# Kernel tuning notes

Measured on AMD Instinct MI355X. Metric: run time of the kernel, lower is better.

Reference implementation:

```python
import jax, jax.numpy as jnp
import numpy as np
from jax import lax

B, C, H, W = 8, 128, 128, 128


def setup_inputs() -> dict:
    key = jax.random.key(0)
    ks = jax.random.split(key, 10)
    s = 0.02
    return {
        "x": jax.random.normal(ks[0], (B, C, H, W), jnp.float32),
        "ln_w": jnp.ones((C,), jnp.float32),
        "ln_b": jnp.zeros((C,), jnp.float32),
        "qkv_w": jax.random.normal(ks[1], (3 * C, C, 1, 1), jnp.float32) * s,
        "qkv_b": jnp.zeros((3 * C,), jnp.float32),
        "dw_w": jax.random.normal(ks[2], (3 * C, 1, 3, 3), jnp.float32) * s,
        "dw_b": jnp.zeros((3 * C,), jnp.float32),
        "proj_w": jax.random.normal(ks[3], (C, C, 1, 1), jnp.float32) * s,
        "proj_b": jnp.zeros((C,), jnp.float32),
        "temp1": jnp.ones((1, 1), jnp.float32),
        "temp2": jnp.ones((1, 1), jnp.float32),
    }


def reference(x, ln_w, ln_b, qkv_w, qkv_b, dw_w, dw_b, proj_w, proj_b, temp1, temp2):
    Cd = x.shape[1]

    def ln(t):  # WithBias LayerNorm over channel dim (unbiased=False var)
        mu = t.mean(axis=1, keepdims=True)
        var = ((t - mu) ** 2).mean(axis=1, keepdims=True)
        return (t - mu) / jnp.sqrt(var + 1e-5) * ln_w[None, :, None, None] + ln_b[None, :, None, None]

    def conv1(t, w, b):  # 1x1 conv
        return jnp.einsum('bchw,oc->bohw', t, w[:, :, 0, 0]) + b[None, :, None, None]

    def dwc(t):  # depthwise 3x3, pad 1
        y = lax.conv_general_dilated(t, dw_w, (1, 1), ((1, 1), (1, 1)),
                                     dimension_numbers=('NCHW', 'OIHW', 'NCHW'),
                                     feature_group_count=t.shape[1])
        return y + dw_b[None, :, None, None]

    def l2n(t):  # F.normalize over last axis, eps=1e-12
        return t / jnp.maximum(jnp.linalg.norm(t, axis=-1, keepdims=True), 1e-12)

    # ---- stage 1: pool over H, attention over W (channel-pooled) ----
    qkv = dwc(conv1(ln(x), qkv_w, qkv_b))
    q1, k1, v1 = qkv[:, :Cd], qkv[:, Cd:2 * Cd], qkv[:, 2 * Cd:]
    q1 = l2n(q1.mean(axis=2)[:, None])           # [B,1,C,W]
    k1 = l2n(k1.max(axis=2)[:, None])            # [B,1,C,W]
    attn1 = jax.nn.softmax(jnp.einsum('bocw,bocv->bowv', q1, k1) * temp1, axis=-1)  # [B,1,W,W]
    out1 = jnp.einsum('bchw,bowv->bchv', v1, attn1)
    out1 = x + conv1(out1, proj_w, proj_b)

    # ---- stage 2: pool over C, attention over H ----
    qkv = dwc(conv1(ln(out1), qkv_w, qkv_b))
    q2, k2, v2 = qkv[:, :Cd], qkv[:, Cd:2 * Cd], qkv[:, 2 * Cd:]
    q2 = l2n(q2.mean(axis=1)[:, None])           # [B,1,H,W]
    k2 = l2n(k2.mean(axis=1)[:, None])           # [B,1,H,W]
    attn2 = jax.nn.softmax(jnp.einsum('bohw,bogw->bohg', q2, k2) * temp2, axis=-1)  # [B,1,H,H]
    out2 = jnp.einsum('bchw,bohg->bcgw', v2, attn2)  # = (v^T @ attn)^T
    out = conv1(out2, proj_w, proj_b) + out1
    return out
```

## Files before the change

### kernel.cpp

```cpp
#include <hip/hip_runtime.h>

typedef __attribute__((ext_vector_type(8))) short bf16x8;
typedef __attribute__((ext_vector_type(4))) float f32x4;
typedef __attribute__((ext_vector_type(4))) unsigned short us4;
typedef __attribute__((ext_vector_type(4))) unsigned int u32x4;

static constexpr int CC = 128, NN = 16384;
static constexpr int O3 = 384;
static constexpr long long CN  = (long long)CC * NN;
static constexpr long long O3N = (long long)O3 * NN;

__device__ __forceinline__ float wave_sum(float v) {
  for (int o = 32; o; o >>= 1) v += __shfl_xor(v, o);
  return v;
}
__device__ __forceinline__ float wave_max(float v) {
  for (int o = 32; o; o >>= 1) v = fmaxf(v, __shfl_xor(v, o));
  return v;
}
__device__ __forceinline__ unsigned short f2bf(float f) {
  unsigned u = __float_as_uint(f);
  u += 0x7FFF + ((u >> 16) & 1);
  return (unsigned short)(u >> 16);
}
__device__ __forceinline__ float bf2f(unsigned short h) {
  return __uint_as_float((unsigned)h << 16);
}

__global__ __launch_bounds__(64) void k_prep(const float* __restrict__ qkvw,
                                             const float* __restrict__ qkvb,
                                             const float* __restrict__ lnw,
                                             const float* __restrict__ lnb,
                                             const float* __restrict__ projw,
                                             unsigned short* __restrict__ Aq,
                                             unsigned short* __restrict__ Ap,
                                             float* __restrict__ Svec,
                                             float* __restrict__ bias2) {
  int o = blockIdx.x, t = threadIdx.x;
  if (o < O3) {
    float w0 = qkvw[o * 128 + t], w1 = qkvw[o * 128 + t + 64];
    unsigned short h0 = f2bf(w0 * lnw[t]), h1 = f2bf(w1 * lnw[t + 64]);
    Aq[o * 128 + t] = h0; Aq[o * 128 + t + 64] = h1;
    float s = wave_sum(bf2f(h0) + bf2f(h1));
    float bs = wave_sum(w0 * lnb[t] + w1 * lnb[t + 64]);
    if (t == 0) { Svec[o] = s; bias2[o] = qkvb[o] + bs; }
  } else {
    int r = o - O3;
    Ap[r * 128 + t] = f2bf(projw[r * 128 + t]);
    Ap[r * 128 + t + 64] = f2bf(projw[r * 128 + t + 64]);
  }
}

__global__ __launch_bounds__(256) void k_stats(const float* __restrict__ in,
                                               float* __restrict__ mu,
                                               float* __restrict__ rs) {
  int p = blockIdx.x * 256 + threadIdx.x;
  int b = p >> 14, n = p & (NN - 1);
  const float* base = in + (size_t)b * CN + n;
  float s1 = 0.f, s2 = 0.f;
#pragma unroll 8
  for (int c = 0; c < CC; ++c) { float v = base[(size_t)c * NN]; s1 += v; s2 += v * v; }
  float m = s1 * (1.f / CC);
  float var = s2 * (1.f / CC) - m * m;
  mu[p] = m;
  rs[p] = rsqrtf(var + 1e-5f);
}

__global__ __launch_bounds__(256) void k_qkv_mfma(
    const float* __restrict__ x, const float* __restrict__ mu, const float* __restrict__ rs,
    const unsigned short* __restrict__ Aq, const float* __restrict__ Svec,
    const float* __restrict__ bias2, unsigned short* __restrict__ out, int b0) {
  __shared__ unsigned short Bs[64 * 136];
  __shared__ unsigned short As[384 * 40];
  int bz = blockIdx.z, bg = b0 + bz;
  int n0 = blockIdx.x * 64;
  int t = threadIdx.x, w = t >> 6, l = t & 63;
  int lr = l & 15, lg = l >> 4;
  const float* xb = x + (size_t)bg * CN + n0;

  {
    int cg = t >> 4, nl = t & 15;
#pragma unroll
    for (int r = 0; r < 8; ++r) {
      int c = r * 16 + cg;
      const float* src = xb + (size_t)c * NN + nl;
#pragma unroll
      for (int q = 0; q < 4; ++q)
        Bs[(nl + q * 16) * 136 + c] = f2bf(src[q * 16]);
    }
  }

  f32x4 acc[6][4];
#pragma unroll
  for (int i = 0; i < 6; ++i)
#pragma unroll
    for (int j = 0; j < 4; ++j) acc[i][j] = (f32x4){0.f, 0.f, 0.f, 0.f};

  const unsigned int* Asrc = (const unsigned int*)Aq;
  unsigned int* Adst = (unsigned int*)As;
  for (int ks = 0; ks < 4; ++ks) {
    __syncthreads();
#pragma unroll
    for (int r = 0; r < 24; ++r) {
      int idx = r * 256 + t;
      int o = idx >> 4, cp = idx & 15;
      Adst[o * 20 + cp] = Asrc[(size_t)o * 64 + ks * 16 + cp];
    }
    __syncthreads();
    bf16x8 bfr[4];
#pragma unroll
    for (int j = 0; j < 4; ++j)
      bfr[j] = *(const bf16x8*)&Bs[(16 * j + lr) * 136 + ks * 32 + lg * 8];
#pragma unroll
    for (int i = 0; i < 6; ++i) {
      bf16x8 afr = *(const bf16x8*)&As[(96 * w + 16 * i + lr) * 40 + lg * 8];
#pragma unroll
      for (int j = 0; j < 4; ++j)
        acc[i][j] = __builtin_amdgcn_mfma_f32_16x16x32_bf16(afr, bfr[j], acc[i][j], 0, 0, 0);
    }
  }

  float rsv[4], muv[4];
#pragma unroll
  for (int j = 0; j < 4; ++j) {
    int n = n0 + 16 * j + lr;
    rsv[j] = rs[(size_t)bg * NN + n];
    muv[j] = mu[(size_t)bg * NN + n];
  }
#pragma unroll
  for (int i = 0; i < 6; ++i) {
    int ob = 96 * w + 16 * i + lg * 4;
    float sv[4], bv[4];
#pragma unroll
    for (int r2 = 0; r2 < 4; ++r2) { sv[r2] = Svec[ob + r2]; bv[r2] = bias2[ob + r2]; }
#pragma unroll
    for (int j = 0; j < 4; ++j) {
      int n = n0 + 16 * j + lr;
      unsigned short* op = out + (size_t)bz * O3N + n;
#pragma unroll
      for (int r2 = 0; r2 < 4; ++r2)
        op[(size_t)(ob + r2) * NN] = f2bf(rsv[j] * (acc[i][j][r2] - muv[j] * sv[r2]) + bv[r2]);
    }
  }
}

__global__ __launch_bounds__(1024) void k_dwc(unsigned short* __restrict__ buf,
                                              const float* __restrict__ dww,
                                              const float* __restrict__ dwb,
                                              float* __restrict__ qm,
                                              float* __restrict__ km,
                                              int b0, int stage) {
  __shared__ unsigned short pl[130 * 144];
  __shared__ float red[32 * 128];
  int o = blockIdx.x, bz = blockIdx.y, bg = b0 + bz;
  int t = threadIdx.x;
  unsigned short* base = buf + (size_t)bz * O3N + (size_t)o * NN;

  for (int i = t; i < 9360; i += 1024) ((unsigned*)pl)[i] = 0u;
  __syncthreads();
#pragma unroll
  for (int r = 0; r < 2; ++r) {
    int idx = r * 1024 + t;
    int row = idx >> 4, c8 = (idx & 15) * 8;
    *(u32x4*)&pl[(row + 1) * 144 + 8 + c8] = *(const u32x4*)&base[row * 128 + c8];
  }
  __syncthreads();

  const float* wg = dww + o * 9;
  float w00 = wg[0], w01 = wg[1], w02 = wg[2];
  float w10 = wg[3], w11 = wg[4], w12 = wg[5];
  float w20 = wg[6], w21 = wg[7], w22 = wg[8];
  float bias = dwb[o];
  int mode = (stage == 0) ? (o < 128 ? 1 : (o < 256 ? 2 : 0)) : 0;
  int hh0 = t >> 5, w0 = (t & 31) * 4;
  float csum[4] = {0.f, 0.f, 0.f, 0.f};
  float cmax[4] = {-1e30f, -1e30f, -1e30f, -1e30f};

#pragma unroll
  for (int g = 0; g < 4; ++g) {
    int h = g * 32 + hh0;
    float a0 = bias, a1 = bias, a2 = bias, a3 = bias;
#pragma unroll
    for (int dr = 0; dr < 3; ++dr) {
      const unsigned short* rp = &pl[(h + dr) * 144];
      us4 cA = *(const us4*)&rp[w0 + 4];
      us4 cB = *(const us4*)&rp[w0 + 8];
      us4 cC = *(const us4*)&rp[w0 + 12];
      float f0 = bf2f(cA[3]), f1 = bf2f(cB[0]), f2 = bf2f(cB[1]);
      float f3 = bf2f(cB[2]), f4 = bf2f(cB[3]), f5 = bf2f(cC[0]);
      float wr0 = (dr == 0) ? w00 : (dr == 1 ? w10 : w20);
      float wr1 = (dr == 0) ? w01 : (dr == 1 ? w11 : w21);
      float wr2 = (dr == 0) ? w02 : (dr == 1 ? w12 : w22);
      a0 += f0 * wr0 + f1 * wr1 + f2 * wr2;
      a1 += f1 * wr0 + f2 * wr1 + f3 * wr2;
      a2 += f2 * wr0 + f3 * wr1 + f4 * wr2;
      a3 += f3 * wr0 + f4 * wr1 + f5 * wr2;
    }
    if (mode == 0) {
      us4 ov;
      ov[0] = f2bf(a0); ov[1] = f2bf(a1); ov[2] = f2bf(a2); ov[3] = f2bf(a3);
      *(us4*)&base[g * 4096 + t * 4] = ov;
    } else if (mode == 1) {
      csum[0] += a0; csum[1] += a1; csum[2] += a2; csum[3] += a3;
    } else {
      cmax[0] = fmaxf(cmax[0], a0); cmax[1] = fmaxf(cmax[1], a1);
      cmax[2] = fmaxf(cmax[2], a2); cmax[3] = fmaxf(cmax[3], a3);
    }
  }

  if (mode) {
    int j = t >> 5;
#pragma unroll
    for (int dx = 0; dx < 4; ++dx)
      red[j * 128 + w0 + dx] = (mode == 1) ? csum[dx] : cmax[dx];
    __syncthreads();
    if (t < 128) {
      float v = red[t];
      if (mode == 1) {
        for (int jj = 1; jj < 32; ++jj) v += red[jj * 128 + t];
        qm[(size_t)bg * NN + o * 128 + t] = v * (1.f / 128.f);
      } else {
        for (int jj = 1; jj < 32; ++jj) v = fmaxf(v, red[jj * 128 + t]);
        km[(size_t)bg * NN + (o - 128) * 128 + t] = v;
      }
    }
  }
}

__global__ __launch_bounds__(256) void k_reduce2(const unsigned short* __restrict__ qkv,
                                                 float* __restrict__ qm, float* __restrict__ km,
                                                 int b0) {
  int bz = blockIdx.y;
  int n = blockIdx.x * 256 + threadIdx.x;
  const unsigned short* base = qkv + (size_t)bz * O3N + n;
  float sq = 0.f, sk = 0.f;
#pragma unroll 4
  for (int c = 0; c < 128; ++c) {
    sq += bf2f(base[(size_t)c * NN]);
    sk += bf2f(base[(size_t)(c + 128) * NN]);
  }
  size_t off = (size_t)(b0 + bz) * NN + n;
  qm[off] = sq * (1.f / 128.f);
  km[off] = sk * (1.f / 128.f);
}

__global__ void k_norm2(float* __restrict__ qm, float* __restrict__ km, int row0) {
  float* buf = blockIdx.y ? km : qm;
  int r = row0 + blockIdx.x, t = threadIdx.x;
  float* p = buf + (size_t)r * 128;
  float v0 = p[t], v1 = p[t + 64];
  float s = wave_sum(v0 * v0 + v1 * v1);
  float sc = 1.f / fmaxf(sqrtf(s), 1e-12f);
  p[t] = v0 * sc;
  p[t + 64] = v1 * sc;
}

__global__ void k_attn1(const float* __restrict__ qm, const float* __restrict__ km,
                        const float* __restrict__ temp, unsigned short* __restrict__ attnT,
                        int b0) {
  int bg = b0 + blockIdx.y;
  int i = blockIdx.x, t = threadIdx.x;
  const float* qb = qm + (size_t)bg * NN;
  const float* kb = km + (size_t)bg * NN;
  __shared__ float qcol[128];
  __shared__ float wred[2];
  qcol[t] = qb[t * 128 + i];
  __syncthreads();
  float s = 0.f;
#pragma unroll 4
  for (int k = 0; k < 128; ++k) s += qcol[k] * kb[k * 128 + t];
  s *= temp[0];
  int wid = t >> 6, lane = t & 63;
  float mx = wave_max(s);
  if (lane == 0) wred[wid] = mx;
  __syncthreads();
  mx = fmaxf(wred[0], wred[1]);
  float pv = __expf(s - mx);
  __syncthreads();
  float sm = wave_sum(pv);
  if (lane == 0) wred[wid] = sm;
  __syncthreads();
  float denom = wred[0] + wred[1];
  attnT[(size_t)bg * NN + (size_t)t * 128 + i] = f2bf(pv / denom);
}

__global__ void k_attn2(const float* __restrict__ qm, const float* __restrict__ km,
                        const float* __restrict__ temp, unsigned short* __restrict__ attnT,
                        int b0) {
  int bg = b0 + blockIdx.y;
  int i = blockIdx.x, t = threadIdx.x;
  const float* qb = qm + (size_t)bg * NN + i * 128;
  const float* kb = km + (size_t)bg * NN + (size_t)t * 128;
  __shared__ float qrow[128];
  __shared__ float wred[2];
  qrow[t] = qb[t];
  __syncthreads();
  float s = 0.f;
#pragma unroll 4
  for (int w = 0; w < 128; ++w) s += qrow[w] * kb[w];
  s *= temp[0];
  int wid = t >> 6, lane = t & 63;
  float mx = wave_max(s);
  if (lane == 0) wred[wid] = mx;
  __syncthreads();
  mx = fmaxf(wred[0], wred[1]);
  float pv = __expf(s - mx);
  __syncthreads();
  float sm = wave_sum(pv);
  if (lane == 0) wred[wid] = sm;
  __syncthreads();
  float denom = wred[0] + wred[1];
  attnT[(size_t)bg * NN + (size_t)t * 128 + i] = f2bf(pv / denom);
}

__global__ __launch_bounds__(256) void k_apply1_mfma(unsigned short* __restrict__ buf,
                                                     const unsigned short* __restrict__ attnT,
                                                     int b0) {
  __shared__ unsigned short Al[128 * 136];
  __shared__ unsigned short Bl[128 * 136];
  int bz = blockIdx.z, bg = b0 + bz;
  int m0 = blockIdx.x * 128;
  int t = threadIdx.x, w = t >> 6, l = t & 63, lr = l & 15, lg = l >> 4;
  const unsigned short* asrc = buf + (size_t)bz * O3N + (size_t)256 * NN + (size_t)m0 * 128;
  const unsigned short* bsrc = attnT + (size_t)bg * NN;
#pragma unroll
  for (int r = 0; r < 8; ++r) {
    int idx = r * 256 + t;
    int row = idx >> 4, c8 = (idx & 15) * 8;
    *(u32x4*)&Al[row * 136 + c8] = *(const u32x4*)&asrc[row * 128 + c8];
    *(u32x4*)&Bl[row * 136 + c8] = *(const u32x4*)&bsrc[row * 128 + c8];
  }
  __syncthreads();
  f32x4 acc[2][8];
#pragma unroll
  for (int i = 0; i < 2; ++i)
#pragma unroll
    for (int j = 0; j < 8; ++j) acc[i][j] = (f32x4){0.f, 0.f, 0.f, 0.f};
#pragma unroll
  for (int ks = 0; ks < 4; ++ks) {
    bf16x8 bfr[8];
#pragma unroll
    for (int j = 0; j < 8; ++j)
      bfr[j] = *(const bf16x8*)&Bl[(16 * j + lr) * 136 + ks * 32 + lg * 8];
#pragma unroll
    for (int i = 0; i < 2; ++i) {
      bf16x8 afr = *(const bf16x8*)&Al[(32 * w + 16 * i + lr) * 136 + ks * 32 + lg * 8];
#pragma unroll
      for (int j = 0; j < 8; ++j)
        acc[i][j] = __builtin_amdgcn_mfma_f32_16x16x32_bf16(afr, bfr[j], acc[i][j], 0, 0, 0);
    }
  }
  unsigned short* ob = buf + (size_t)bz * O3N;
#pragma unroll
  for (int i = 0; i < 2; ++i)
#pragma unroll
    for (int j = 0; j < 8; ++j)
#pragma unroll
      for (int r2 = 0; r2 < 4; ++r2) {
        int m = m0 + 32 * w + 16 * i + lg * 4 + r2;
        int n = 16 * j + lr;
        ob[(size_t)m * 128 + n] = f2bf(acc[i][j][r2]);
      }
}

__global__ __launch_bounds__(256) void k_apply2_mfma(unsigned short* __restrict__ buf,
                                                     const unsigned short* __restrict__ attnT,
                                                     int b0) {
  __shared__ unsigned short At[128 * 136];
  __shared__ unsigned short Bt[128 * 136];
  int bz = blockIdx.z, bg = b0 + bz, c = blockIdx.x;
  int t = threadIdx.x, w = t >> 6, l = t & 63, lr = l & 15, lg = l >> 4;
  const unsigned short* vsrc = buf + (size_t)bz * O3N + (size_t)(256 + c) * NN;
  const unsigned short* asrc = attnT + (size_t)bg * NN;
#pragma unroll
  for (int r = 0; r < 8; ++r) {
    int idx = r * 256 + t;
    int row = idx >> 4, c8 = (idx & 15) * 8;
    *(u32x4*)&At[row * 136 + c8] = *(const u32x4*)&asrc[row * 128 + c8];
    us4 lo = *(const us4*)&vsrc[row * 128 + c8];
    us4 hi = *(const us4*)&vsrc[row * 128 + c8 + 4];
#pragma unroll
    for (int q = 0; q < 4; ++q) {
      Bt[(c8 + q) * 136 + row] = lo[q];
      Bt[(c8 + 4 + q) * 136 + row] = hi[q];
    }
  }
  __syncthreads();
  f32x4 acc[2][8];
#pragma unroll
  for (int i = 0; i < 2; ++i)
#pragma unroll
    for (int j = 0; j < 8; ++j) acc[i][j] = (f32x4){0.f, 0.f, 0.f, 0.f};
#pragma unroll
  for (int ks = 0; ks < 4; ++ks) {
    bf16x8 bfr[8];
#pragma unroll
    for (int j = 0; j < 8; ++j)
      bfr[j] = *(const bf16x8*)&Bt[(16 * j + lr) * 136 + ks * 32 + lg * 8];
#pragma unroll
    for (int i = 0; i < 2; ++i) {
      bf16x8 afr = *(const bf16x8*)&At[(32 * w + 16 * i + lr) * 136 + ks * 32 + lg * 8];
#pragma unroll
      for (int j = 0; j < 8; ++j)
        acc[i][j] = __builtin_amdgcn_mfma_f32_16x16x32_bf16(afr, bfr[j], acc[i][j], 0, 0, 0);
    }
  }
  unsigned short* ob = buf + (size_t)bz * O3N + (size_t)c * NN;
#pragma unroll
  for (int i = 0; i < 2; ++i)
#pragma unroll
    for (int j = 0; j < 8; ++j)
#pragma unroll
      for (int r2 = 0; r2 < 4; ++r2) {
        int g = 32 * w + 16 * i + lg * 4 + r2;
        int n = 16 * j + lr;
        ob[(size_t)g * 128 + n] = f2bf(acc[i][j][r2]);
      }
}

__global__ __launch_bounds__(256) void k_proj_mfma(
    const unsigned short* __restrict__ tin, const unsigned short* __restrict__ Ap,
    const float* __restrict__ pb, const float* __restrict__ res,
    float* __restrict__ dst, float* __restrict__ mu, float* __restrict__ rs,
    int b0, int do_stats) {
  __shared__ unsigned short Al[128 * 136];
  __shared__ unsigned short Bs2[64 * 136];
  __shared__ float red1[64 * 17];
  __shared__ float red2[64 * 17];
  int bz = blockIdx.z, bg = b0 + bz;
  int n0 = blockIdx.x * 64;
  int t = threadIdx.x, w = t >> 6, l = t & 63, lr = l & 15, lg = l >> 4;
  const unsigned short* tb = tin + (size_t)bz * O3N;
#pragma unroll
  for (int r = 0; r < 8; ++r) {
    int idx = r * 256 + t;
    int row = idx >> 4, c8 = (idx & 15) * 8;
    *(u32x4*)&Al[row * 136 + c8] = *(const u32x4*)&Ap[row * 128 + c8];
  }
#pragma unroll
  for (int r = 0; r < 32; ++r) {
    int idx = r * 256 + t;
    int cI = idx >> 6, nI = idx & 63;
    Bs2[nI * 136 + cI] = tb[(size_t)cI * NN + n0 + nI];
  }
  __syncthreads();

  f32x4 acc[2][4];
#pragma unroll
  for (int i = 0; i < 2; ++i)
#pragma unroll
    for (int j = 0; j < 4; ++j) acc[i][j] = (f32x4){0.f, 0.f, 0.f, 0.f};
#pragma unroll
  for (int ks = 0; ks < 4; ++ks) {
    bf16x8 bfr[4];
#pragma unroll
    for (int j = 0; j < 4; ++j)
      bfr[j] = *(const bf16x8*)&Bs2[(16 * j + lr) * 136 + ks * 32 + lg * 8];
#pragma unroll
    for (int i = 0; i < 2; ++i) {
      bf16x8 afr = *(const bf16x8*)&Al[(32 * w + 16 * i + lr) * 136 + ks * 32 + lg * 8];
#pragma unroll
      for (int j = 0; j < 4; ++j)
        acc[i][j] = __builtin_amdgcn_mfma_f32_16x16x32_bf16(afr, bfr[j], acc[i][j], 0, 0, 0);
    }
  }

  float s1p[4] = {0.f, 0.f, 0.f, 0.f}, s2p[4] = {0.f, 0.f, 0.f, 0.f};
#pragma unroll
  for (int i = 0; i < 2; ++i) {
    int ob = 32 * w + 16 * i + lg * 4;
    float bv[4];
#pragma unroll
    for (int r2 = 0; r2 < 4; ++r2) bv[r2] = pb[ob + r2];
#pragma unroll
    for (int j = 0; j < 4; ++j) {
      int n = n0 + 16 * j + lr;
#pragma unroll
      for (int r2 = 0; r2 < 4; ++r2) {
        size_t off = (size_t)bg * CN + (size_t)(ob + r2) * NN + n;
        float val = acc[i][j][r2] + bv[r2] + res[off];
        dst[off] = val;
        s1p[j] += val;
        s2p[j] += val * val;
      }
    }
  }
  if (do_stats) {
#pragma unroll
    for (int j = 0; j < 4; ++j) {
      red1[(16 * j + lr) * 17 + (w * 4 + lg)] = s1p[j];
      red2[(16 * j + lr) * 17 + (w * 4 + lg)] = s2p[j];
    }
    __syncthreads();
    if (t < 64) {
      float s1 = 0.f, s2 = 0.f;
#pragma unroll
      for (int kk = 0; kk < 16; ++kk) { s1 += red1[t * 17 + kk]; s2 += red2[t * 17 + kk]; }
      float m = s1 * (1.f / 128.f);
      float var = s2 * (1.f / 128.f) - m * m;
      mu[(size_t)bg * NN + n0 + t] = m;
      rs[(size_t)bg * NN + n0 + t] = rsqrtf(var + 1e-5f);
    }
  }
}

extern "C" void kernel_launch(void* const* d_in, const int* in_sizes, int n_in,
                              void* d_out, int out_size, void* d_ws, size_t ws_size,
                              hipStream_t stream) {
  (void)in_sizes; (void)n_in; (void)out_size;
  const float* x     = (const float*)d_in[0];
  const float* lnw   = (const float*)d_in[1];
  const float* lnb   = (const float*)d_in[2];
  const float* qkvw  = (const float*)d_in[3];
  const float* qkvb  = (const float*)d_in[4];
  const float* dww   = (const float*)d_in[5];
  const float* dwb   = (const float*)d_in[6];
  const float* projw = (const float*)d_in[7];
  const float* projb = (const float*)d_in[8];
  const float* temp1 = (const float*)d_in[9];
  const float* temp2 = (const float*)d_in[10];
  float* out = (float*)d_out;
  float* ws = (float*)d_ws;

  auto needBytes = [&](int nb) {
    return ((size_t)nb * (O3N / 2) + 4ull * 131072 + 65536 + 768 + 24576 + 8192) * 4;
  };
  int NB = 8;
  while (NB > 1 && ws_size < needBytes(NB)) NB >>= 1;
  if (ws_size < needBytes(1)) return;

  unsigned short* convbuf = (unsigned short*)ws;
  float* mu = ws + (size_t)NB * (O3N / 2);
  float* rs = mu + 131072;
  float* qm = rs + 131072;
  float* km = qm + 131072;
  unsigned short* attnT = (unsigned short*)(km + 131072);
  float* Svec  = (float*)(attnT + 8ull * NN);
  float* bias2 = Svec + 384;
  unsigned short* Aq = (unsigned short*)(bias2 + 384);
  unsigned short* Ap = Aq + 49152;

  k_prep<<<512, 64, 0, stream>>>(qkvw, qkvb, lnw, lnb, projw, Aq, Ap, Svec, bias2);
  k_stats<<<512, 256, 0, stream>>>(x, mu, rs);

  for (int stage = 0; stage < 2; ++stage) {
    const float* src = stage ? out : x;
    for (int b0 = 0; b0 < 8; b0 += NB) {
      k_qkv_mfma<<<dim3(256, 1, NB), 256, 0, stream>>>(src, mu, rs, Aq, Svec, bias2, convbuf, b0);
      k_dwc<<<dim3(384, NB), 1024, 0, stream>>>(convbuf, dww, dwb, qm, km, b0, stage);
      if (stage == 1)
        k_reduce2<<<dim3(64, NB), 256, 0, stream>>>(convbuf, qm, km, b0);
      k_norm2<<<dim3(NB * 128, 2), 64, 0, stream>>>(qm, km, b0 * 128);
      if (stage == 0)
        k_attn1<<<dim3(128, NB), 128, 0, stream>>>(qm, km, temp1, attnT, b0);
      else
        k_attn2<<<dim3(128, NB), 128, 0, stream>>>(qm, km, temp2, attnT, b0);
      if (stage == 0)
        k_apply1_mfma<<<dim3(128, 1, NB), 256, 0, stream>>>(convbuf, attnT, b0);
      else
        k_apply2_mfma<<<dim3(128, 1, NB), 256, 0, stream>>>(convbuf, attnT, b0);
      const float* resp = stage ? out : x;
      k_proj_mfma<<<dim3(256, 1, NB), 256, 0, stream>>>(convbuf, Ap, projb, resp, out,
                                                        mu, rs, b0, stage == 0 ? 1 : 0);
    }
  }
}
```

Measured before the change: 319.6 us.

## Load GEMM weights directly from global, swizzle LDS B tile, trim dwc zeroing

In the QKV and projection MFMA kernels, the weight fragments are now read directly from global memory (cached in L1/L2) instead of being staged through shared memory. This removes the per-k-step syncthreads and the A-tile LDS traffic. The B tile is built with packed 16-byte LDS writes into an XOR-swizzled, unpadded layout, replacing scattered 2-byte stores. The depthwise-conv kernel now zeroes only the halo border of its padded plane rather than the whole buffer. The trade-off is more global or L2 load latency on the A operand inside the MFMA loop, and lower LDS use, which may allow higher occupancy.

```diff
diff --git a/kernel.cpp b/kernel.cpp
--- a/kernel.cpp
+++ b/kernel.cpp
@@ -70,8 +70,7 @@
     const float* __restrict__ x, const float* __restrict__ mu, const float* __restrict__ rs,
     const unsigned short* __restrict__ Aq, const float* __restrict__ Svec,
     const float* __restrict__ bias2, unsigned short* __restrict__ out, int b0) {
-  __shared__ unsigned short Bs[64 * 136];
-  __shared__ unsigned short As[384 * 40];
+  __shared__ unsigned short Bs[64 * 128];
   int bz = blockIdx.z, bg = b0 + bz;
   int n0 = blockIdx.x * 64;
   int t = threadIdx.x, w = t >> 6, l = t & 63;
@@ -79,16 +78,22 @@
   const float* xb = x + (size_t)bg * CN + n0;
 
   {
-    int cg = t >> 4, nl = t & 15;
-#pragma unroll
-    for (int r = 0; r < 8; ++r) {
-      int c = r * 16 + cg;
-      const float* src = xb + (size_t)c * NN + nl;
-#pragma unroll
-      for (int q = 0; q < 4; ++q)
-        Bs[(nl + q * 16) * 136 + c] = f2bf(src[q * 16]);
-    }
-  }
+    int n = t & 63, cb = t >> 6;
+#pragma unroll
+    for (int g = 0; g < 4; ++g) {
+      int c8 = (cb * 4 + g) * 8;
+      unsigned pk[4];
+#pragma unroll
+      for (int q = 0; q < 4; ++q) {
+        unsigned short a = f2bf(xb[(size_t)(c8 + 2 * q) * NN + n]);
+        unsigned short b = f2bf(xb[(size_t)(c8 + 2 * q + 1) * NN + n]);
+        pk[q] = (unsigned)a | ((unsigned)b << 16);
+      }
+      int c8s = c8 ^ ((n & 7) << 3);
+      *(u32x4*)&Bs[n * 128 + c8s] = *(const u32x4*)pk;
+    }
+  }
+  __syncthreads();
 
   f32x4 acc[6][4];
 #pragma unroll
@@ -96,24 +101,19 @@
 #pragma unroll
     for (int j = 0; j < 4; ++j) acc[i][j] = (f32x4){0.f, 0.f, 0.f, 0.f};
 
-  const unsigned int* Asrc = (const unsigned int*)Aq;
-  unsigned int* Adst = (unsigned int*)As;
+  const unsigned short* Abase = Aq + (size_t)(96 * w + lr) * 128 + lg * 8;
+#pragma unroll
   for (int ks = 0; ks < 4; ++ks) {
-    __syncthreads();
-#pragma unroll
-    for (int r = 0; r < 24; ++r) {
-      int idx = r * 256 + t;
-      int o = idx >> 4, cp = idx & 15;
-      Adst[o * 20 + cp] = Asrc[(size_t)o * 64 + ks * 16 + cp];
-    }
-    __syncthreads();
     bf16x8 bfr[4];
 #pragma unroll
-    for (int j = 0; j < 4; ++j)
-      bfr[j] = *(const bf16x8*)&Bs[(16 * j + lr) * 136 + ks * 32 + lg * 8];
+    for (int j = 0; j < 4; ++j) {
+      int row = 16 * j + lr;
+      int col = (ks * 32 + lg * 8) ^ ((lr & 7) << 3);
+      bfr[j] = *(const bf16x8*)&Bs[row * 128 + col];
+    }
 #pragma unroll
     for (int i = 0; i < 6; ++i) {
-      bf16x8 afr = *(const bf16x8*)&As[(96 * w + 16 * i + lr) * 40 + lg * 8];
+      bf16x8 afr = *(const bf16x8*)&Abase[(size_t)(16 * i) * 128 + ks * 32];
 #pragma unroll
       for (int j = 0; j < 4; ++j)
         acc[i][j] = __builtin_amdgcn_mfma_f32_16x16x32_bf16(afr, bfr[j], acc[i][j], 0, 0, 0);
@@ -155,8 +155,16 @@
   int o = blockIdx.x, bz = blockIdx.y, bg = b0 + bz;
   int t = threadIdx.x;
   unsigned short* base = buf + (size_t)bz * O3N + (size_t)o * NN;
-
-  for (int i = t; i < 9360; i += 1024) ((unsigned*)pl)[i] = 0u;
+  unsigned* pl32 = (unsigned*)pl;
+
+  for (int i = t; i < 1168; i += 1024) {
+    int idx;
+    if (i < 72) idx = i;
+    else if (i < 144) idx = 129 * 72 + (i - 72);
+    else { int j = i - 144; int row = (j >> 3) + 1; int s = j & 7;
+           idx = row * 72 + (s < 4 ? s : 64 + s); }
+    pl32[idx] = 0u;
+  }
   __syncthreads();
 #pragma unroll
   for (int r = 0; r < 2; ++r) {
@@ -423,25 +431,29 @@
     const float* __restrict__ pb, const float* __restrict__ res,
     float* __restrict__ dst, float* __restrict__ mu, float* __restrict__ rs,
     int b0, int do_stats) {
-  __shared__ unsigned short Al[128 * 136];
-  __shared__ unsigned short Bs2[64 * 136];
+  __shared__ unsigned short Bs2[64 * 128];
   __shared__ float red1[64 * 17];
   __shared__ float red2[64 * 17];
   int bz = blockIdx.z, bg = b0 + bz;
   int n0 = blockIdx.x * 64;
   int t = threadIdx.x, w = t >> 6, l = t & 63, lr = l & 15, lg = l >> 4;
-  const unsigned short* tb = tin + (size_t)bz * O3N;
-#pragma unroll
-  for (int r = 0; r < 8; ++r) {
-    int idx = r * 256 + t;
-    int row = idx >> 4, c8 = (idx & 15) * 8;
-    *(u32x4*)&Al[row * 136 + c8] = *(const u32x4*)&Ap[row * 128 + c8];
-  }
-#pragma unroll
-  for (int r = 0; r < 32; ++r) {
-    int idx = r * 256 + t;
-    int cI = idx >> 6, nI = idx & 63;
-    Bs2[nI * 136 + cI] = tb[(size_t)cI * NN + n0 + nI];
+  const unsigned short* tb = tin + (size_t)bz * O3N + n0;
+
+  {
+    int n = t & 63, cb = t >> 6;
+#pragma unroll
+    for (int g = 0; g < 4; ++g) {
+      int c8 = (cb * 4 + g) * 8;
+      unsigned pk[4];
+#pragma unroll
+      for (int q = 0; q < 4; ++q) {
+        unsigned short a = tb[(size_t)(c8 + 2 * q) * NN + n];
+        unsigned short b = tb[(size_t)(c8 + 2 * q + 1) * NN + n];
+        pk[q] = (unsigned)a | ((unsigned)b << 16);
+      }
+      int c8s = c8 ^ ((n & 7) << 3);
+      *(u32x4*)&Bs2[n * 128 + c8s] = *(const u32x4*)pk;
+    }
   }
   __syncthreads();
 
@@ -450,15 +462,20 @@
   for (int i = 0; i < 2; ++i)
 #pragma unroll
     for (int j = 0; j < 4; ++j) acc[i][j] = (f32x4){0.f, 0.f, 0.f, 0.f};
+
+  const unsigned short* Abase = Ap + (size_t)(32 * w + lr) * 128 + lg * 8;
 #pragma unroll
   for (int ks = 0; ks < 4; ++ks) {
     bf16x8 bfr[4];
 #pragma unroll
-    for (int j = 0; j < 4; ++j)
-      bfr[j] = *(const bf16x8*)&Bs2[(16 * j + lr) * 136 + ks * 32 + lg * 8];
+    for (int j = 0; j < 4; ++j) {
+      int row = 16 * j + lr;
+      int col = (ks * 32 + lg * 8) ^ ((lr & 7) << 3);
+      bfr[j] = *(const bf16x8*)&Bs2[row * 128 + col];
+    }
 #pragma unroll
     for (int i = 0; i < 2; ++i) {
-      bf16x8 afr = *(const bf16x8*)&Al[(32 * w + 16 * i + lr) * 136 + ks * 32 + lg * 8];
+      bf16x8 afr = *(const bf16x8*)&Abase[(size_t)(16 * i) * 128 + ks * 32];
 #pragma unroll
       for (int j = 0; j < 4; ++j)
         acc[i][j] = __builtin_amdgcn_mfma_f32_16x16x32_bf16(afr, bfr[j], acc[i][j], 0, 0, 0);
```

After: 338.8 us. +6.0%, slower.
